# Performance work log

Measured on AMD Instinct MI355X. Metric: run time of the kernel, lower is better.

The kernel has to match this reference:

```python
import jax, jax.numpy as jnp
import numpy as np

ITERS = 20
EPS = 1e-6

def setup_inputs() -> dict:
    key = jax.random.key(0)
    logits = jax.random.normal(key, (128, 64, 64, 64), dtype=jnp.float32)
    return {"logits": logits}

def reference(logits) -> jnp.ndarray:
    # Per-(H,W) matrix: stabilized exp over rows, then 20 Sinkhorn iterations.
    x = logits.astype(jnp.float32)
    # row-wise max (over W, last axis), matching tl.max(x, axis=1)
    x = jnp.exp(x - jnp.max(x, axis=-1, keepdims=True))

    def body(i, x):
        row_sum = jnp.sum(x, axis=-1, keepdims=True)   # sum over W
        x = x / (row_sum + EPS)
        col_sum = jnp.sum(x, axis=-2, keepdims=True)   # sum over H
        x = x / (col_sum + EPS)
        return x

    x = jax.lax.fori_loop(0, ITERS, body, x)
    return x
```

## Files before the change

### kernel.cpp

```cpp
#include <hip/hip_runtime.h>


static constexpr int   kIters = 20;
static constexpr float kEps   = 1e-6f;

__device__ __forceinline__ float RLf(float x, int l) {
    return __int_as_float(__builtin_amdgcn_readlane(__float_as_int(x), l));
}

__global__ __launch_bounds__(128) void sinkhorn64_split(const float* __restrict__ in,
                                                        float* __restrict__ out) {
    __shared__ float xb0[2][64];
    __shared__ float xb1[2][64];
    const int tid  = threadIdx.x;
    const int h    = tid >> 6;
    const int lane = tid & 63;
    const int c    = (lane + 32 * h) & 63;
    const long m   = blockIdx.x;
    const float* __restrict__ A = in  + m * 4096;
    float* __restrict__ O       = out + m * 4096;

    float cK[32];
#pragma unroll
    for (int i = 0; i < 32; ++i) cK[i] = A[((32 * h + i) << 6) + lane];

    float rK[32];
#pragma unroll
    for (int k4 = 0; k4 < 8; ++k4) {
        const float4 f = *reinterpret_cast<const float4*>(A + (lane << 6) + 32 * h + (k4 << 2));
        rK[4 * k4 + 0] = f.x; rK[4 * k4 + 1] = f.y;
        rK[4 * k4 + 2] = f.z; rK[4 * k4 + 3] = f.w;
    }

    float pm = rK[0];
#pragma unroll
    for (int k = 1; k < 32; ++k) pm = fmaxf(pm, rK[k]);
    xb0[h][lane] = pm;
    __syncthreads();
    const float mx  = fmaxf(pm, xb0[1 - h][lane]);
    const float mxr = fmaxf(xb0[0][c], xb0[1][c]);

#pragma unroll
    for (int k = 0; k < 32; ++k) rK[k] = __expf(rK[k] - mx);
#pragma unroll
    for (int i = 0; i < 32; ++i) cK[i] = __expf(cK[i] - RLf(mxr, i));

    float ur = 1.0f, vr = 1.0f;

#pragma unroll 1
    for (int it = 0; it < kIters; ++it) {
        float a0 = 0.f, a1 = 0.f, a2 = 0.f, a3 = 0.f;
#pragma unroll
        for (int k = 0; k < 32; k += 4) {
            a0 = fmaf(RLf(vr, k + 0), rK[k + 0], a0);
            a1 = fmaf(RLf(vr, k + 1), rK[k + 1], a1);
            a2 = fmaf(RLf(vr, k + 2), rK[k + 2], a2);
            a3 = fmaf(RLf(vr, k + 3), rK[k + 3], a3);
        }
        xb1[h][lane] = (a0 + a1) + (a2 + a3);
        __syncthreads();
        const float w = xb1[0][c] + xb1[1][c];
        ur = ur * __builtin_amdgcn_rcpf(fmaf(ur, w, kEps));

        float b0 = 0.f, b1 = 0.f, b2 = 0.f, b3 = 0.f;
#pragma unroll
        for (int i = 0; i < 32; i += 4) {
            b0 = fmaf(RLf(ur, i + 0), cK[i + 0], b0);
            b1 = fmaf(RLf(ur, i + 1), cK[i + 1], b1);
            b2 = fmaf(RLf(ur, i + 2), cK[i + 2], b2);
            b3 = fmaf(RLf(ur, i + 3), cK[i + 3], b3);
        }
        xb0[h][lane] = (b0 + b1) + (b2 + b3);
        __syncthreads();
        const float t = xb0[0][c] + xb0[1][c];
        vr = vr * __builtin_amdgcn_rcpf(fmaf(vr, t, kEps));
    }

    xb1[h][lane] = vr;
    __syncthreads();
    const float vfin = xb1[0][lane];

#pragma unroll
    for (int i = 0; i < 32; ++i) {
        O[((32 * h + i) << 6) + lane] = RLf(ur, i) * cK[i] * vfin;
    }
}

extern "C" void kernel_launch(void* const* d_in, const int* in_sizes, int n_in,
                              void* d_out, int out_size, void* d_ws, size_t ws_size,
                              hipStream_t stream) {
    const float* in = (const float*)d_in[0];
    float* out      = (float*)d_out;
    sinkhorn64_split<<<8192, 128, 0, stream>>>(in, out);
}
```

Baseline: 89.99 us.

## Process two Sinkhorn matrices per block to interleave independent work

Each 128-thread block now handles two 64x64 matrices instead of one, and the grid shrinks to half as many blocks. The readlane/FMA chains for both matrices are interleaved, and the two matrices share each barrier, so each barrier is amortized over twice the work. This gives the scheduler independent instructions to hide readlane and FMA latency. The cost is roughly double the register use (128+ values per thread for the two K copies), which is capped by launch_bounds(128,3) and may lower occupancy or cause spills.

```diff
diff --git a/kernel.cpp b/kernel.cpp
--- a/kernel.cpp
+++ b/kernel.cpp
@@ -8,81 +8,119 @@
     return __int_as_float(__builtin_amdgcn_readlane(__float_as_int(x), l));
 }
 
-__global__ __launch_bounds__(128) void sinkhorn64_split(const float* __restrict__ in,
+__global__ __launch_bounds__(128, 3) void sinkhorn64_x2(const float* __restrict__ in,
                                                         float* __restrict__ out) {
-    __shared__ float xb0[2][64];
-    __shared__ float xb1[2][64];
+    __shared__ float xA0[2][64], xA1[2][64];
+    __shared__ float xB0[2][64], xB1[2][64];
     const int tid  = threadIdx.x;
     const int h    = tid >> 6;
     const int lane = tid & 63;
     const int c    = (lane + 32 * h) & 63;
-    const long m   = blockIdx.x;
-    const float* __restrict__ A = in  + m * 4096;
-    float* __restrict__ O       = out + m * 4096;
+    const long m0  = (long)blockIdx.x * 2;
+    const float* __restrict__ A0 = in  + m0 * 4096;
+    const float* __restrict__ A1 = A0 + 4096;
+    float* __restrict__ O0       = out + m0 * 4096;
+    float* __restrict__ O1       = O0 + 4096;
 
-    float cK[32];
+    float cK0[32], cK1[32];
 #pragma unroll
-    for (int i = 0; i < 32; ++i) cK[i] = A[((32 * h + i) << 6) + lane];
+    for (int i = 0; i < 32; ++i) cK0[i] = A0[((32 * h + i) << 6) + lane];
+#pragma unroll
+    for (int i = 0; i < 32; ++i) cK1[i] = A1[((32 * h + i) << 6) + lane];
 
-    float rK[32];
+    float rK0[32], rK1[32];
 #pragma unroll
     for (int k4 = 0; k4 < 8; ++k4) {
-        const float4 f = *reinterpret_cast<const float4*>(A + (lane << 6) + 32 * h + (k4 << 2));
-        rK[4 * k4 + 0] = f.x; rK[4 * k4 + 1] = f.y;
-        rK[4 * k4 + 2] = f.z; rK[4 * k4 + 3] = f.w;
+        const float4 f = *reinterpret_cast<const float4*>(A0 + (lane << 6) + 32 * h + (k4 << 2));
+        rK0[4 * k4 + 0] = f.x; rK0[4 * k4 + 1] = f.y;
+        rK0[4 * k4 + 2] = f.z; rK0[4 * k4 + 3] = f.w;
+    }
+#pragma unroll
+    for (int k4 = 0; k4 < 8; ++k4) {
+        const float4 f = *reinterpret_cast<const float4*>(A1 + (lane << 6) + 32 * h + (k4 << 2));
+        rK1[4 * k4 + 0] = f.x; rK1[4 * k4 + 1] = f.y;
+        rK1[4 * k4 + 2] = f.z; rK1[4 * k4 + 3] = f.w;
     }
 
-    float pm = rK[0];
+    float p0 = rK0[0], p1 = rK1[0];
 #pragma unroll
-    for (int k = 1; k < 32; ++k) pm = fmaxf(pm, rK[k]);
-    xb0[h][lane] = pm;
+    for (int k = 1; k < 32; ++k) { p0 = fmaxf(p0, rK0[k]); p1 = fmaxf(p1, rK1[k]); }
+    xA0[h][lane] = p0;
+    xB0[h][lane] = p1;
     __syncthreads();
-    const float mx  = fmaxf(pm, xb0[1 - h][lane]);
-    const float mxr = fmaxf(xb0[0][c], xb0[1][c]);
+    const float mx0 = fmaxf(p0, xA0[1 - h][lane]);
+    const float mr0 = fmaxf(xA0[0][c], xA0[1][c]);
+    const float mx1 = fmaxf(p1, xB0[1 - h][lane]);
+    const float mr1 = fmaxf(xB0[0][c], xB0[1][c]);
 
 #pragma unroll
-    for (int k = 0; k < 32; ++k) rK[k] = __expf(rK[k] - mx);
+    for (int k = 0; k < 32; ++k) {
+        rK0[k] = __expf(rK0[k] - mx0);
+        rK1[k] = __expf(rK1[k] - mx1);
+    }
 #pragma unroll
-    for (int i = 0; i < 32; ++i) cK[i] = __expf(cK[i] - RLf(mxr, i));
+    for (int i = 0; i < 32; ++i) {
+        cK0[i] = __expf(cK0[i] - RLf(mr0, i));
+        cK1[i] = __expf(cK1[i] - RLf(mr1, i));
+    }
 
-    float ur = 1.0f, vr = 1.0f;
+    float u0 = 1.0f, v0 = 1.0f, u1 = 1.0f, v1 = 1.0f;
 
 #pragma unroll 1
     for (int it = 0; it < kIters; ++it) {
         float a0 = 0.f, a1 = 0.f, a2 = 0.f, a3 = 0.f;
+        float b0 = 0.f, b1 = 0.f, b2 = 0.f, b3 = 0.f;
 #pragma unroll
         for (int k = 0; k < 32; k += 4) {
-            a0 = fmaf(RLf(vr, k + 0), rK[k + 0], a0);
-            a1 = fmaf(RLf(vr, k + 1), rK[k + 1], a1);
-            a2 = fmaf(RLf(vr, k + 2), rK[k + 2], a2);
-            a3 = fmaf(RLf(vr, k + 3), rK[k + 3], a3);
+            a0 = fmaf(RLf(v0, k + 0), rK0[k + 0], a0);
+            b0 = fmaf(RLf(v1, k + 0), rK1[k + 0], b0);
+            a1 = fmaf(RLf(v0, k + 1), rK0[k + 1], a1);
+            b1 = fmaf(RLf(v1, k + 1), rK1[k + 1], b1);
+            a2 = fmaf(RLf(v0, k + 2), rK0[k + 2], a2);
+            b2 = fmaf(RLf(v1, k + 2), rK1[k + 2], b2);
+            a3 = fmaf(RLf(v0, k + 3), rK0[k + 3], a3);
+            b3 = fmaf(RLf(v1, k + 3), rK1[k + 3], b3);
         }
-        xb1[h][lane] = (a0 + a1) + (a2 + a3);
+        xA1[h][lane] = (a0 + a1) + (a2 + a3);
+        xB1[h][lane] = (b0 + b1) + (b2 + b3);
         __syncthreads();
-        const float w = xb1[0][c] + xb1[1][c];
-        ur = ur * __builtin_amdgcn_rcpf(fmaf(ur, w, kEps));
+        const float w0 = xA1[0][c] + xA1[1][c];
+        u0 = u0 * __builtin_amdgcn_rcpf(fmaf(u0, w0, kEps));
+        const float w1 = xB1[0][c] + xB1[1][c];
+        u1 = u1 * __builtin_amdgcn_rcpf(fmaf(u1, w1, kEps));
 
-        float b0 = 0.f, b1 = 0.f, b2 = 0.f, b3 = 0.f;
+        float d0 = 0.f, d1 = 0.f, d2 = 0.f, d3 = 0.f;
+        float e0 = 0.f, e1 = 0.f, e2 = 0.f, e3 = 0.f;
 #pragma unroll
         for (int i = 0; i < 32; i += 4) {
-            b0 = fmaf(RLf(ur, i + 0), cK[i + 0], b0);
-            b1 = fmaf(RLf(ur, i + 1), cK[i + 1], b1);
-            b2 = fmaf(RLf(ur, i + 2), cK[i + 2], b2);
-            b3 = fmaf(RLf(ur, i + 3), cK[i + 3], b3);
+            d0 = fmaf(RLf(u0, i + 0), cK0[i + 0], d0);
+            e0 = fmaf(RLf(u1, i + 0), cK1[i + 0], e0);
+            d1 = fmaf(RLf(u0, i + 1), cK0[i + 1], d1);
+            e1 = fmaf(RLf(u1, i + 1), cK1[i + 1], e1);
+            d2 = fmaf(RLf(u0, i + 2), cK0[i + 2], d2);
+            e2 = fmaf(RLf(u1, i + 2), cK1[i + 2], e2);
+            d3 = fmaf(RLf(u0, i + 3), cK0[i + 3], d3);
+            e3 = fmaf(RLf(u1, i + 3), cK1[i + 3], e3);
         }
-        xb0[h][lane] = (b0 + b1) + (b2 + b3);
+        xA0[h][lane] = (d0 + d1) + (d2 + d3);
+        xB0[h][lane] = (e0 + e1) + (e2 + e3);
         __syncthreads();
-        const float t = xb0[0][c] + xb0[1][c];
-        vr = vr * __builtin_amdgcn_rcpf(fmaf(vr, t, kEps));
+        const float t0 = xA0[0][c] + xA0[1][c];
+        v0 = v0 * __builtin_amdgcn_rcpf(fmaf(v0, t0, kEps));
+        const float t1 = xB0[0][c] + xB0[1][c];
+        v1 = v1 * __builtin_amdgcn_rcpf(fmaf(v1, t1, kEps));
     }
 
-    xb1[h][lane] = vr;
+    xA1[h][lane] = v0;
+    xB1[h][lane] = v1;
     __syncthreads();
-    const float vfin = xb1[0][lane];
+    const float vf0 = xA1[0][lane];
+    const float vf1 = xB1[0][lane];
 
 #pragma unroll
     for (int i = 0; i < 32; ++i) {
-        O[((32 * h + i) << 6) + lane] = RLf(ur, i) * cK[i] * vfin;
+        O0[((32 * h + i) << 6) + lane] = RLf(u0, i) * cK0[i] * vf0;
+        O1[((32 * h + i) << 6) + lane] = RLf(u1, i) * cK1[i] * vf1;
     }
 }
 
@@ -91,5 +129,5 @@
                               hipStream_t stream) {
     const float* in = (const float*)d_in[0];
     float* out      = (float*)d_out;
-    sinkhorn64_split<<<8192, 128, 0, stream>>>(in, out);
+    sinkhorn64_x2<<<4096, 128, 0, stream>>>(in, out);
 }
```

After: 123.4 us. +37.1%, slower.

## Split each 64x64 Sinkhorn matrix across four wavefronts instead of two

Applied to the files above, without the earlier changes.

Each block now uses 256 threads (four wavefronts), and each wavefront holds a 16-row and 16-column quarter of the matrix in registers instead of a 32-wide half. Partial row and column sums are exchanged through transposed shared buffers and read back as one float4 per thread. This halves the serial readlane/FMA chain per iteration and the register footprint per thread, at the cost of more wavefronts hitting each barrier and more LDS traffic.

```diff
diff --git a/kernel.cpp b/kernel.cpp
--- a/kernel.cpp
+++ b/kernel.cpp
@@ -8,81 +8,86 @@
     return __int_as_float(__builtin_amdgcn_readlane(__float_as_int(x), l));
 }
 
-__global__ __launch_bounds__(128) void sinkhorn64_split(const float* __restrict__ in,
-                                                        float* __restrict__ out) {
-    __shared__ float xb0[2][64];
-    __shared__ float xb1[2][64];
+__global__ __launch_bounds__(256) void sinkhorn64_q4(const float* __restrict__ in,
+                                                     float* __restrict__ out) {
+    __shared__ __align__(16) float xbW[64][4];
+    __shared__ __align__(16) float xbT[64][4];
+    __shared__ float vbuf[64];
     const int tid  = threadIdx.x;
-    const int h    = tid >> 6;
+    const int q    = tid >> 6;
     const int lane = tid & 63;
-    const int c    = (lane + 32 * h) & 63;
+    const int c    = (lane + 16 * q) & 63;
     const long m   = blockIdx.x;
     const float* __restrict__ A = in  + m * 4096;
     float* __restrict__ O       = out + m * 4096;
 
-    float cK[32];
+    float cK[16];
 #pragma unroll
-    for (int i = 0; i < 32; ++i) cK[i] = A[((32 * h + i) << 6) + lane];
+    for (int i = 0; i < 16; ++i) cK[i] = A[((16 * q + i) << 6) + lane];
 
-    float rK[32];
+    float rK[16];
 #pragma unroll
-    for (int k4 = 0; k4 < 8; ++k4) {
-        const float4 f = *reinterpret_cast<const float4*>(A + (lane << 6) + 32 * h + (k4 << 2));
+    for (int k4 = 0; k4 < 4; ++k4) {
+        const float4 f = *reinterpret_cast<const float4*>(A + (lane << 6) + 16 * q + (k4 << 2));
         rK[4 * k4 + 0] = f.x; rK[4 * k4 + 1] = f.y;
         rK[4 * k4 + 2] = f.z; rK[4 * k4 + 3] = f.w;
     }
 
     float pm = rK[0];
 #pragma unroll
-    for (int k = 1; k < 32; ++k) pm = fmaxf(pm, rK[k]);
-    xb0[h][lane] = pm;
+    for (int k = 1; k < 16; ++k) pm = fmaxf(pm, rK[k]);
+    xbT[lane][q] = pm;
     __syncthreads();
-    const float mx  = fmaxf(pm, xb0[1 - h][lane]);
-    const float mxr = fmaxf(xb0[0][c], xb0[1][c]);
+    const float4 f4 = *reinterpret_cast<const float4*>(xbT[lane]);
+    const float  mx = fmaxf(fmaxf(f4.x, f4.y), fmaxf(f4.z, f4.w));
+    const float4 g4 = *reinterpret_cast<const float4*>(xbT[c]);
+    const float mxc = fmaxf(fmaxf(g4.x, g4.y), fmaxf(g4.z, g4.w));
 
 #pragma unroll
-    for (int k = 0; k < 32; ++k) rK[k] = __expf(rK[k] - mx);
+    for (int k = 0; k < 16; ++k) rK[k] = __expf(rK[k] - mx);
 #pragma unroll
-    for (int i = 0; i < 32; ++i) cK[i] = __expf(cK[i] - RLf(mxr, i));
+    for (int i = 0; i < 16; ++i) cK[i] = __expf(cK[i] - RLf(mxc, i));
 
-    float ur = 1.0f, vr = 1.0f;
+    float u = 1.0f, v = 1.0f;
 
 #pragma unroll 1
     for (int it = 0; it < kIters; ++it) {
         float a0 = 0.f, a1 = 0.f, a2 = 0.f, a3 = 0.f;
 #pragma unroll
-        for (int k = 0; k < 32; k += 4) {
-            a0 = fmaf(RLf(vr, k + 0), rK[k + 0], a0);
-            a1 = fmaf(RLf(vr, k + 1), rK[k + 1], a1);
-            a2 = fmaf(RLf(vr, k + 2), rK[k + 2], a2);
-            a3 = fmaf(RLf(vr, k + 3), rK[k + 3], a3);
+        for (int k = 0; k < 16; k += 4) {
+            a0 = fmaf(RLf(v, k + 0), rK[k + 0], a0);
+            a1 = fmaf(RLf(v, k + 1), rK[k + 1], a1);
+            a2 = fmaf(RLf(v, k + 2), rK[k + 2], a2);
+            a3 = fmaf(RLf(v, k + 3), rK[k + 3], a3);
         }
-        xb1[h][lane] = (a0 + a1) + (a2 + a3);
+        xbW[lane][q] = (a0 + a1) + (a2 + a3);
         __syncthreads();
-        const float w = xb1[0][c] + xb1[1][c];
-        ur = ur * __builtin_amdgcn_rcpf(fmaf(ur, w, kEps));
+        const float4 w4 = *reinterpret_cast<const float4*>(xbW[c]);
+        const float  w  = (w4.x + w4.y) + (w4.z + w4.w);
+        u = u * __builtin_amdgcn_rcpf(fmaf(u, w, kEps));
 
         float b0 = 0.f, b1 = 0.f, b2 = 0.f, b3 = 0.f;
 #pragma unroll
-        for (int i = 0; i < 32; i += 4) {
-            b0 = fmaf(RLf(ur, i + 0), cK[i + 0], b0);
-            b1 = fmaf(RLf(ur, i + 1), cK[i + 1], b1);
-            b2 = fmaf(RLf(ur, i + 2), cK[i + 2], b2);
-            b3 = fmaf(RLf(ur, i + 3), cK[i + 3], b3);
+        for (int i = 0; i < 16; i += 4) {
+            b0 = fmaf(RLf(u, i + 0), cK[i + 0], b0);
+            b1 = fmaf(RLf(u, i + 1), cK[i + 1], b1);
+            b2 = fmaf(RLf(u, i + 2), cK[i + 2], b2);
+            b3 = fmaf(RLf(u, i + 3), cK[i + 3], b3);
         }
-        xb0[h][lane] = (b0 + b1) + (b2 + b3);
+        xbT[lane][q] = (b0 + b1) + (b2 + b3);
         __syncthreads();
-        const float t = xb0[0][c] + xb0[1][c];
-        vr = vr * __builtin_amdgcn_rcpf(fmaf(vr, t, kEps));
+        const float4 t4 = *reinterpret_cast<const float4*>(xbT[c]);
+        const float  t  = (t4.x + t4.y) + (t4.z + t4.w);
+        v = v * __builtin_amdgcn_rcpf(fmaf(v, t, kEps));
     }
 
-    xb1[h][lane] = vr;
+    vbuf[c] = v;
     __syncthreads();
-    const float vfin = xb1[0][lane];
+    const float vf = vbuf[lane];
 
 #pragma unroll
-    for (int i = 0; i < 32; ++i) {
-        O[((32 * h + i) << 6) + lane] = RLf(ur, i) * cK[i] * vfin;
+    for (int i = 0; i < 16; ++i) {
+        O[((16 * q + i) << 6) + lane] = RLf(u, i) * cK[i] * vf;
     }
 }
 
@@ -91,5 +96,5 @@
                               hipStream_t stream) {
     const float* in = (const float*)d_in[0];
     float* out      = (float*)d_out;
-    sinkhorn64_split<<<8192, 128, 0, stream>>>(in, out);
+    sinkhorn64_q4<<<8192, 256, 0, stream>>>(in, out);
 }
```

Measured after the change: 96.47 us. 1.07x slower.
